# Kernel tuning notes

Hardware: AMD Instinct MI355X
Metric: run time of the kernel (lower is better)

## Reference

```python
import jax, jax.numpy as jnp
import numpy as np

N = 50000    # nodes
E = 800000   # edges (avg degree 16)
H = 4        # attention heads
IN = 128     # input feature size
HID = 128    # hidden size per head
OUT = 64     # output size per head
GAT_SLOPE = 0.2   # DGL GATConv internal LeakyReLU slope
ACT_SLOPE = 0.01  # nn.LeakyReLU default slope


def _lrelu(x, s):
    return jnp.where(x >= 0, x, s * x)


def _gat_conv(x, src, dst, W, attn_l, attn_r, bias, heads, out_dim):
    """DGL GATConv (feat_drop disabled for deterministic reference).
    x: [N, F_in] -> out: [N, heads, out_dim]"""
    z = (x @ W).reshape(N, heads, out_dim)                 # [N,H,D]
    el = jnp.sum(z * attn_l, axis=-1)                      # [N,H]
    er = jnp.sum(z * attn_r, axis=-1)                      # [N,H]
    e = _lrelu(el[src] + er[dst], GAT_SLOPE)               # [E,H]
    # edge softmax over incoming edges of each dst node (numerically stable)
    emax = jax.ops.segment_max(e, dst, num_segments=N)     # [N,H]
    ex = jnp.exp(e - emax[dst])                            # [E,H]
    esum = jax.ops.segment_sum(ex, dst, num_segments=N)    # [N,H]
    alpha = ex / esum[dst]                                 # [E,H]
    msg = alpha[:, :, None] * z[src]                       # [E,H,D]
    out = jax.ops.segment_sum(msg, dst, num_segments=N)    # [N,H,D]
    return out + bias.reshape(1, heads, out_dim)


def setup_inputs() -> dict:
    key = jax.random.key(0)
    ks = jax.random.split(key, 20)
    def nrm(k, shape, scale=0.05):
        return jax.random.normal(k, shape, dtype=jnp.float32) * scale
    return {
        "n_feat": jax.random.normal(ks[0], (N, IN), dtype=jnp.float32),
        "src": jax.random.randint(ks[1], (E,), 0, N),
        "dst": jax.random.randint(ks[2], (E,), 0, N),
        # input GATConv: IN -> HID x H
        "g0_W": nrm(ks[3], (IN, H * HID)),
        "g0_al": nrm(ks[4], (H, HID)),
        "g0_ar": nrm(ks[5], (H, HID)),
        "g0_b": jnp.zeros((H * HID,), jnp.float32),
        "d0_W": nrm(ks[6], (HID, H * HID)),
        "d0_b": jnp.zeros((HID,), jnp.float32),
        # middle GATConv: HID -> HID x H
        "g1_W": nrm(ks[7], (HID, H * HID)),
        "g1_al": nrm(ks[8], (H, HID)),
        "g1_ar": nrm(ks[9], (H, HID)),
        "g1_b": jnp.zeros((H * HID,), jnp.float32),
        "d1_W": nrm(ks[10], (HID, H * HID)),
        "d1_b": jnp.zeros((HID,), jnp.float32),
        # output GATConv: HID -> OUT x H
        "g2_W": nrm(ks[11], (HID, H * OUT)),
        "g2_al": nrm(ks[12], (H, OUT)),
        "g2_ar": nrm(ks[13], (H, OUT)),
        "g2_b": jnp.zeros((H * OUT,), jnp.float32),
    }


def reference(n_feat, src, dst,
              g0_W, g0_al, g0_ar, g0_b, d0_W, d0_b,
              g1_W, g1_al, g1_ar, g1_b, d1_W, d1_b,
              g2_W, g2_al, g2_ar, g2_b):
    # input GAT + dense
    h = _gat_conv(n_feat, src, dst, g0_W, g0_al, g0_ar, g0_b, H, HID)  # [N,H,HID]
    h = _lrelu(h, ACT_SLOPE).reshape(N, H * HID)
    h = _lrelu(h @ d0_W.T + d0_b, ACT_SLOPE)                            # [N,HID]
    # middle GAT + dense
    h = _gat_conv(h, src, dst, g1_W, g1_al, g1_ar, g1_b, H, HID)
    h = _lrelu(h, ACT_SLOPE).reshape(N, H * HID)
    h = _lrelu(h @ d1_W.T + d1_b, ACT_SLOPE)                            # [N,HID]
    # output GAT, mean over heads
    h = _gat_conv(h, src, dst, g2_W, g2_al, g2_ar, g2_b, H, OUT)        # [N,H,OUT]
    h = _lrelu(h, ACT_SLOPE)
    h = jnp.mean(h, axis=-2)                                            # [N,OUT]
    h = _lrelu(h, ACT_SLOPE)
    return h
```

## Files before the change

kernel.cpp:

```cpp
#include <hip/hip_runtime.h>

#define NN 50000
#define EE 800000
#define HH 4

typedef __attribute__((ext_vector_type(8))) short short8v;
typedef __attribute__((ext_vector_type(4))) float f32x4;
typedef __attribute__((ext_vector_type(8))) unsigned short ushort8v;
typedef __attribute__((ext_vector_type(4))) unsigned short ushort4v;

__device__ __forceinline__ float b2f(unsigned short u) {
    return __uint_as_float(((unsigned int)u) << 16);
}
__device__ __forceinline__ unsigned short f2b(float f) {
    unsigned int x = __float_as_uint(f);
    x += 0x7fffu + ((x >> 16) & 1u);
    return (unsigned short)(x >> 16);
}

template<int WR, bool ACT, int WEL>
__global__ __launch_bounds__(256) void mgemm_k(
    const unsigned short* __restrict__ A, const unsigned short* __restrict__ Bt,
    const float* __restrict__ bias, unsigned short* __restrict__ C,
    const float* __restrict__ al, const float* __restrict__ ar,
    float* __restrict__ el, float* __restrict__ er,
    int M, int N, int K, float slope)
{
    constexpr int BM = 64 * WR;
    __shared__ unsigned short As[BM * 72];
    __shared__ unsigned short Bs[128 * 72];
    const int t   = threadIdx.x;
    const int m0  = blockIdx.y * BM;
    const int n0  = blockIdx.x * 128;
    const int w   = t >> 6;
    const int l   = t & 63;
    const int lr  = l & 15;
    const int lk8 = (l >> 4) * 8;
    const int wbase = w * 16 * WR;

    f32x4 acc[WR][8];
    #pragma unroll
    for (int rr = 0; rr < WR; ++rr)
        #pragma unroll
        for (int i = 0; i < 8; ++i) acc[rr][i] = (f32x4)0.f;

    for (int k0 = 0; k0 < K; k0 += 64) {
        #pragma unroll
        for (int cc = 0; cc < 2 * WR; ++cc) {
            int c = t + cc * 256;
            int row = c >> 3, seg = (c & 7) * 8;
            int gm = m0 + row;
            short8v v = (short8v)0;
            if (gm < M)
                v = *reinterpret_cast<const short8v*>(&A[(size_t)gm * K + k0 + seg]);
            *reinterpret_cast<short8v*>(&As[row * 72 + seg]) = v;
        }
        #pragma unroll
        for (int cc = 0; cc < 4; ++cc) {
            int c = t + cc * 256;
            int row = c >> 3, seg = (c & 7) * 8;
            short8v v = *reinterpret_cast<const short8v*>(
                &Bt[(size_t)(n0 + row) * K + k0 + seg]);
            *reinterpret_cast<short8v*>(&Bs[row * 72 + seg]) = v;
        }
        __syncthreads();
        #pragma unroll
        for (int kk = 0; kk < 64; kk += 32) {
            short8v a[WR];
            #pragma unroll
            for (int rr = 0; rr < WR; ++rr)
                a[rr] = *reinterpret_cast<const short8v*>(
                    &As[(wbase + rr * 16 + lr) * 72 + kk + lk8]);
            #pragma unroll
            for (int nb = 0; nb < 8; ++nb) {
                short8v b = *reinterpret_cast<const short8v*>(
                    &Bs[(nb * 16 + lr) * 72 + kk + lk8]);
                #pragma unroll
                for (int rr = 0; rr < WR; ++rr)
                    acc[rr][nb] = __builtin_amdgcn_mfma_f32_16x16x32_bf16(
                        a[rr], b, acc[rr][nb], 0, 0, 0);
            }
        }
        __syncthreads();
    }

    if (WEL > 0) {
        const int nbh = (WEL == 1) ? 8 : 4;
        const int Dd  = (WEL == 1) ? 128 : 64;
        #pragma unroll
        for (int hh = 0; hh < WEL; ++hh) {
            int head = (WEL == 1) ? blockIdx.x : blockIdx.x * 2 + hh;
            #pragma unroll
            for (int rr = 0; rr < WR; ++rr) {
                float pl[4] = {}, pr[4] = {};
                #pragma unroll
                for (int nb = 0; nb < nbh; ++nb) {
                    float alv = al[head * Dd + nb * 16 + lr];
                    float arv = ar[head * Dd + nb * 16 + lr];
                    #pragma unroll
                    for (int r = 0; r < 4; ++r) {
                        float z = acc[rr][hh * nbh + nb][r];
                        pl[r] = fmaf(z, alv, pl[r]);
                        pr[r] = fmaf(z, arv, pr[r]);
                    }
                }
                #pragma unroll
                for (int r = 0; r < 4; ++r) {
                    #pragma unroll
                    for (int o = 1; o < 16; o <<= 1) {
                        pl[r] += __shfl_xor(pl[r], o);
                        pr[r] += __shfl_xor(pr[r], o);
                    }
                }
                if (lr == 0) {
                    #pragma unroll
                    for (int r = 0; r < 4; ++r) {
                        int gm = m0 + wbase + rr * 16 + (l >> 4) * 4 + r;
                        if (gm < M) {
                            el[gm * HH + head] = pl[r];
                            er[gm * HH + head] = pr[r];
                        }
                    }
                }
            }
        }
    }

    #pragma unroll
    for (int rr = 0; rr < WR; ++rr) {
        #pragma unroll
        for (int nb = 0; nb < 8; ++nb) {
            #pragma unroll
            for (int r = 0; r < 4; ++r) {
                int gm = m0 + wbase + rr * 16 + (l >> 4) * 4 + r;
                int gn = n0 + nb * 16 + lr;
                if (gm < M) {
                    float v = acc[rr][nb][r];
                    if (ACT) { v += bias[gn]; v = v >= 0.f ? v : slope * v; }
                    C[(size_t)gm * N + gn] = f2b(v);
                }
            }
        }
    }
}

__global__ void tr_k(const float* __restrict__ W, unsigned short* __restrict__ Wt,
                     int K, int N)
{
    int idx = blockIdx.x * blockDim.x + threadIdx.x;
    if (idx >= K * N) return;
    int n = idx / K, k = idx - n * K;
    Wt[idx] = f2b(W[(size_t)k * N + n]);
}

__global__ void cast_k(const float* __restrict__ x, unsigned short* __restrict__ y,
                       int n4)
{
    int i = blockIdx.x * blockDim.x + threadIdx.x;
    if (i >= n4) return;
    float4 v = reinterpret_cast<const float4*>(x)[i];
    ushort4v u;
    u[0] = f2b(v.x); u[1] = f2b(v.y); u[2] = f2b(v.z); u[3] = f2b(v.w);
    reinterpret_cast<ushort4v*>(y)[i] = u;
}

__global__ void hist_k(const int* __restrict__ dst, int* __restrict__ cnt)
{
    int i = blockIdx.x * blockDim.x + threadIdx.x;
    if (i < EE) atomicAdd(&cnt[dst[i]], 1);
}

#define SCAN_B 196
__global__ __launch_bounds__(256) void scan1_k(const int* __restrict__ cnt,
                                               int* __restrict__ offs,
                                               int* __restrict__ bsum)
{
    __shared__ int sh[256];
    int b = blockIdx.x, t = threadIdx.x, i = b * 256 + t;
    int v = (i < NN) ? cnt[i] : 0;
    sh[t] = v;
    __syncthreads();
    #pragma unroll
    for (int o = 1; o < 256; o <<= 1) {
        int add = (t >= o) ? sh[t - o] : 0;
        __syncthreads();
        sh[t] += add;
        __syncthreads();
    }
    if (i < NN) offs[i] = sh[t] - v;
    if (t == 255) bsum[b] = sh[t];
}

__global__ __launch_bounds__(256) void scan2_k(int* __restrict__ bsum)
{
    __shared__ int sh[256];
    int t = threadIdx.x;
    int v = (t < SCAN_B) ? bsum[t] : 0;
    sh[t] = v;
    __syncthreads();
    #pragma unroll
    for (int o = 1; o < 256; o <<= 1) {
        int add = (t >= o) ? sh[t - o] : 0;
        __syncthreads();
        sh[t] += add;
        __syncthreads();
    }
    if (t < SCAN_B) bsum[t] = sh[t] - v;
}

__global__ __launch_bounds__(256) void scan3_k(int* __restrict__ offs,
                                               const int* __restrict__ bsum)
{
    int b = blockIdx.x, t = threadIdx.x, i = b * 256 + t;
    if (i < NN) offs[i] += bsum[b];
    if (i == NN - 1) offs[NN] = EE;
}

__global__ void scatter_k(const int* __restrict__ src, const int* __restrict__ dst,
                          const int* __restrict__ offs, int* __restrict__ cursor,
                          int* __restrict__ srcs_sorted)
{
    int i = blockIdx.x * blockDim.x + threadIdx.x;
    if (i >= EE) return;
    int d = dst[i];
    int p = offs[d] + atomicAdd(&cursor[d], 1);
    srcs_sorted[p] = src[i];
}

template<int D, bool MEAN>
__global__ __launch_bounds__(256) void agg2_k(
    const unsigned short* __restrict__ zb, const float* __restrict__ el,
    const float* __restrict__ er, const int* __restrict__ offs,
    const int* __restrict__ srcs, const float* __restrict__ bias,
    unsigned short* __restrict__ outb, float* __restrict__ outf)
{
    constexpr int HD  = HH * D;
    constexpr int EPL = HD / 64;
    typedef __attribute__((ext_vector_type(EPL))) unsigned short uvec;
    int n = blockIdx.x * 4 + (threadIdx.x >> 6);
    if (n >= NN) return;
    int lane = threadIdx.x & 63;
    int h = lane >> 4;
    int beg = offs[n];
    int cnt_e = offs[n + 1] - beg;
    float erh = er[n * HH + h];

    float acc[EPL] = {};
    float wsum = 0.f;

    if (cnt_e > 0) {
        auto LD = [&](int idx, uvec& v, float& elv) {
            int e = idx < cnt_e ? idx : cnt_e - 1;
            int s = srcs[beg + e];
            elv = el[s * HH + h];
            v = *reinterpret_cast<const uvec*>(&zb[(size_t)s * HD + lane * EPL]);
        };
        auto PROC = [&](const uvec& v, float elv) {
            float x = elv + erh;
            x = x >= 0.f ? x : 0.2f * x;
            float ex = __expf(x);
            wsum += ex;
            #pragma unroll
            for (int j = 0; j < EPL; ++j)
                acc[j] = fmaf(ex, b2f(v[j]), acc[j]);
        };
        uvec v0, v1, v2, v3;
        float e0, e1, e2, e3;
        LD(0, v0, e0); LD(1, v1, e1); LD(2, v2, e2); LD(3, v3, e3);
        for (int c0 = 0; c0 < cnt_e; c0 += 4) {
            PROC(v0, e0); LD(c0 + 4, v0, e0);
            if (c0 + 1 < cnt_e) { PROC(v1, e1); } LD(c0 + 5, v1, e1);
            if (c0 + 2 < cnt_e) { PROC(v2, e2); } LD(c0 + 6, v2, e2);
            if (c0 + 3 < cnt_e) { PROC(v3, e3); } LD(c0 + 7, v3, e3);
        }
    }
    float inv = wsum > 0.f ? 1.f / wsum : 0.f;

    float vv[EPL];
    #pragma unroll
    for (int j = 0; j < EPL; ++j) {
        float v = acc[j] * inv + bias[h * D + (lane & 15) * EPL + j];
        vv[j] = v >= 0.f ? v : 0.01f * v;
    }

    if (!MEAN) {
        uvec u;
        #pragma unroll
        for (int j = 0; j < EPL; ++j) u[j] = f2b(vv[j]);
        *reinterpret_cast<uvec*>(&outb[(size_t)n * HD + lane * EPL]) = u;
    } else {
        #pragma unroll
        for (int j = 0; j < EPL; ++j) {
            float s = vv[j];
            s += __shfl_xor(s, 16);
            s += __shfl_xor(s, 32);
            s *= 0.25f;
            vv[j] = s >= 0.f ? s : 0.01f * s;
        }
        if (lane < 16) {
            float* op = outf + (size_t)n * D + lane * EPL;
            #pragma unroll
            for (int j = 0; j < EPL; j += 4)
                *reinterpret_cast<float4*>(op + j) =
                    make_float4(vv[j], vv[j + 1], vv[j + 2], vv[j + 3]);
        }
    }
}

extern "C" void kernel_launch(void* const* d_in, const int* in_sizes, int n_in,
                              void* d_out, int out_size, void* d_ws, size_t ws_size,
                              hipStream_t stream)
{
    const float* n_feat = (const float*)d_in[0];
    const int*   src    = (const int*)d_in[1];
    const int*   dst    = (const int*)d_in[2];
    const float* g0_W  = (const float*)d_in[3];
    const float* g0_al = (const float*)d_in[4];
    const float* g0_ar = (const float*)d_in[5];
    const float* g0_b  = (const float*)d_in[6];
    const float* d0_W  = (const float*)d_in[7];
    const float* d0_b  = (const float*)d_in[8];
    const float* g1_W  = (const float*)d_in[9];
    const float* g1_al = (const float*)d_in[10];
    const float* g1_ar = (const float*)d_in[11];
    const float* g1_b  = (const float*)d_in[12];
    const float* d1_W  = (const float*)d_in[13];
    const float* d1_b  = (const float*)d_in[14];
    const float* g2_W  = (const float*)d_in[15];
    const float* g2_al = (const float*)d_in[16];
    const float* g2_ar = (const float*)d_in[17];
    const float* g2_b  = (const float*)d_in[18];

    char* ws = (char*)d_ws;
    size_t off = 0;
    auto alloc = [&](size_t bytes) {
        void* p = ws + off;
        off += (bytes + 255) & ~(size_t)255;
        return p;
    };
    unsigned short* zB   = (unsigned short*)alloc((size_t)NN * 512 * 2);
    unsigned short* hB   = (unsigned short*)alloc((size_t)NN * 512 * 2);
    unsigned short* hC   = (unsigned short*)alloc((size_t)NN * 128 * 2);
    unsigned short* xF   = (unsigned short*)alloc((size_t)NN * 128 * 2);
    unsigned short* g0t  = (unsigned short*)alloc(512 * 128 * 2);
    unsigned short* g1t  = (unsigned short*)alloc(512 * 128 * 2);
    unsigned short* g2t  = (unsigned short*)alloc(256 * 128 * 2);
    unsigned short* d0t  = (unsigned short*)alloc(128 * 512 * 2);
    unsigned short* d1t  = (unsigned short*)alloc(128 * 512 * 2);
    float*          el   = (float*)alloc((size_t)NN * HH * 4);
    float*          er   = (float*)alloc((size_t)NN * HH * 4);
    int*            cnt  = (int*)alloc((size_t)NN * 4);
    int*            curs = (int*)alloc((size_t)NN * 4);
    int*            offs = (int*)alloc((size_t)(NN + 1) * 4);
    int*            srcs = (int*)alloc((size_t)EE * 4);
    int*            bsum = (int*)alloc(256 * 4);

    hipMemsetAsync(cnt, 0, (size_t)NN * 4, stream);
    hipMemsetAsync(curs, 0, (size_t)NN * 4, stream);
    hist_k<<<(EE + 255) / 256, 256, 0, stream>>>(dst, cnt);
    scan1_k<<<SCAN_B, 256, 0, stream>>>(cnt, offs, bsum);
    scan2_k<<<1, 256, 0, stream>>>(bsum);
    scan3_k<<<SCAN_B, 256, 0, stream>>>(offs, bsum);
    scatter_k<<<(EE + 255) / 256, 256, 0, stream>>>(src, dst, offs, curs, srcs);

    cast_k<<<(NN * 128 / 4 + 255) / 256, 256, 0, stream>>>(n_feat, xF, NN * 128 / 4);
    cast_k<<<(128 * 512 / 4 + 255) / 256, 256, 0, stream>>>(d0_W, d0t, 128 * 512 / 4);
    cast_k<<<(128 * 512 / 4 + 255) / 256, 256, 0, stream>>>(d1_W, d1t, 128 * 512 / 4);
    tr_k<<<(128 * 512 + 255) / 256, 256, 0, stream>>>(g0_W, g0t, 128, 512);
    tr_k<<<(128 * 512 + 255) / 256, 256, 0, stream>>>(g1_W, g1t, 128, 512);
    tr_k<<<(128 * 256 + 255) / 256, 256, 0, stream>>>(g2_W, g2t, 128, 256);

    const int MT   = (NN + 63) / 64;
    const int MT2  = (NN + 127) / 128;
    const int NODB = (NN + 3) / 4;

    mgemm_k<2, false, 1><<<dim3(4, MT2), 256, 0, stream>>>(
        xF, g0t, nullptr, zB, g0_al, g0_ar, el, er, NN, 512, 128, 0.f);
    agg2_k<128, false><<<NODB, 256, 0, stream>>>(zB, el, er, offs, srcs, g0_b,
                                                 hB, nullptr);
    mgemm_k<1, true, 0><<<dim3(1, MT), 256, 0, stream>>>(
        hB, d0t, d0_b, hC, nullptr, nullptr, nullptr, nullptr, NN, 128, 512, 0.01f);

    mgemm_k<2, false, 1><<<dim3(4, MT2), 256, 0, stream>>>(
        hC, g1t, nullptr, zB, g1_al, g1_ar, el, er, NN, 512, 128, 0.f);
    agg2_k<128, false><<<NODB, 256, 0, stream>>>(zB, el, er, offs, srcs, g1_b,
                                                 hB, nullptr);
    mgemm_k<1, true, 0><<<dim3(1, MT), 256, 0, stream>>>(
        hB, d1t, d1_b, hC, nullptr, nullptr, nullptr, nullptr, NN, 128, 512, 0.01f);

    mgemm_k<2, false, 2><<<dim3(2, MT2), 256, 0, stream>>>(
        hC, g2t, nullptr, zB, g2_al, g2_ar, el, er, NN, 256, 128, 0.f);
    agg2_k<64, true><<<NODB, 256, 0, stream>>>(zB, el, er, offs, srcs, g2_b,
                                               nullptr, (float*)d_out);
}
```

Measured before the change: 570.7 us.

## Store GAT features head-major and aggregate one head per block for cache locality

The projection GEMM now writes z in a head-major layout [H][N][128] and el/er as [H][N], and the first two aggregations launch a separate grid slice per head. Each wave then gathers 256-byte rows from one head's table. The working set per head is smaller and more likely to stay in L2/MALL while the random neighbour gathers run. In exchange each head pass rereads the CSR offsets and source indices and reruns the exp/softmax weight math separately, and each edge now issues smaller loads.

```diff
diff --git a/kernel.cpp b/kernel.cpp
--- a/kernel.cpp
+++ b/kernel.cpp
@@ -6,7 +6,6 @@
 
 typedef __attribute__((ext_vector_type(8))) short short8v;
 typedef __attribute__((ext_vector_type(4))) float f32x4;
-typedef __attribute__((ext_vector_type(8))) unsigned short ushort8v;
 typedef __attribute__((ext_vector_type(4))) unsigned short ushort4v;
 
 __device__ __forceinline__ float b2f(unsigned short u) {
@@ -18,12 +17,12 @@
     return (unsigned short)(x >> 16);
 }
 
-template<int WR, bool ACT, int WEL>
+template<int WR, bool ACT, int WEL, bool HS>
 __global__ __launch_bounds__(256) void mgemm_k(
     const unsigned short* __restrict__ A, const unsigned short* __restrict__ Bt,
     const float* __restrict__ bias, unsigned short* __restrict__ C,
     const float* __restrict__ al, const float* __restrict__ ar,
-    float* __restrict__ el, float* __restrict__ er,
+    float* __restrict__ elt, float* __restrict__ ert,
     int M, int N, int K, float slope)
 {
     constexpr int BM = 64 * WR;
@@ -117,8 +116,8 @@
                     for (int r = 0; r < 4; ++r) {
                         int gm = m0 + wbase + rr * 16 + (l >> 4) * 4 + r;
                         if (gm < M) {
-                            el[gm * HH + head] = pl[r];
-                            er[gm * HH + head] = pr[r];
+                            elt[(size_t)head * NN + gm] = pl[r];
+                            ert[(size_t)head * NN + gm] = pr[r];
                         }
                     }
                 }
@@ -137,7 +136,13 @@
                 if (gm < M) {
                     float v = acc[rr][nb][r];
                     if (ACT) { v += bias[gn]; v = v >= 0.f ? v : slope * v; }
-                    C[(size_t)gm * N + gn] = f2b(v);
+                    if (HS) {
+                        int head = blockIdx.x;
+                        int d = nb * 16 + lr;
+                        C[((size_t)head * NN + gm) * 128 + d] = f2b(v);
+                    } else {
+                        C[(size_t)gm * N + gn] = f2b(v);
+                    }
                 }
             }
         }
@@ -227,15 +232,64 @@
     srcs_sorted[p] = src[i];
 }
 
-template<int D, bool MEAN>
-__global__ __launch_bounds__(256) void agg2_k(
-    const unsigned short* __restrict__ zb, const float* __restrict__ el,
-    const float* __restrict__ er, const int* __restrict__ offs,
+__global__ __launch_bounds__(256) void agg3_k(
+    const unsigned short* __restrict__ zh, const float* __restrict__ elt,
+    const float* __restrict__ ert, const int* __restrict__ offs,
     const int* __restrict__ srcs, const float* __restrict__ bias,
-    unsigned short* __restrict__ outb, float* __restrict__ outf)
-{
-    constexpr int HD  = HH * D;
-    constexpr int EPL = HD / 64;
+    unsigned short* __restrict__ outb)
+{
+    int n = blockIdx.x * 4 + (threadIdx.x >> 6);
+    if (n >= NN) return;
+    int h = blockIdx.y;
+    int lane = threadIdx.x & 63;
+    int beg = offs[n];
+    int cnt_e = offs[n + 1] - beg;
+    float erh = ert[(size_t)h * NN + n];
+    const unsigned short* ztab = zh + (size_t)h * NN * 128;
+    const float* elh = elt + (size_t)h * NN;
+
+    float a0 = 0.f, a1 = 0.f, wsum = 0.f;
+    if (cnt_e > 0) {
+        auto LD = [&](int idx, unsigned int& v, float& elv) {
+            int e = idx < cnt_e ? idx : cnt_e - 1;
+            int s = srcs[beg + e];
+            elv = elh[s];
+            v = *reinterpret_cast<const unsigned int*>(&ztab[(size_t)s * 128 + lane * 2]);
+        };
+        auto PROC = [&](unsigned int v, float elv) {
+            float x = elv + erh;
+            x = x >= 0.f ? x : 0.2f * x;
+            float ex = __expf(x);
+            wsum += ex;
+            a0 = fmaf(ex, b2f((unsigned short)(v & 0xffff)), a0);
+            a1 = fmaf(ex, b2f((unsigned short)(v >> 16)), a1);
+        };
+        unsigned int v0, v1, v2, v3;
+        float e0, e1, e2, e3;
+        LD(0, v0, e0); LD(1, v1, e1); LD(2, v2, e2); LD(3, v3, e3);
+        for (int c0 = 0; c0 < cnt_e; c0 += 4) {
+            PROC(v0, e0); LD(c0 + 4, v0, e0);
+            if (c0 + 1 < cnt_e) { PROC(v1, e1); } LD(c0 + 5, v1, e1);
+            if (c0 + 2 < cnt_e) { PROC(v2, e2); } LD(c0 + 6, v2, e2);
+            if (c0 + 3 < cnt_e) { PROC(v3, e3); } LD(c0 + 7, v3, e3);
+        }
+    }
+    float inv = wsum > 0.f ? 1.f / wsum : 0.f;
+    float x0 = a0 * inv + bias[h * 128 + lane * 2];
+    float x1 = a1 * inv + bias[h * 128 + lane * 2 + 1];
+    x0 = x0 >= 0.f ? x0 : 0.01f * x0;
+    x1 = x1 >= 0.f ? x1 : 0.01f * x1;
+    unsigned int u = (unsigned int)f2b(x0) | ((unsigned int)f2b(x1) << 16);
+    *reinterpret_cast<unsigned int*>(&outb[(size_t)n * 512 + h * 128 + lane * 2]) = u;
+}
+
+__global__ __launch_bounds__(256) void aggm_k(
+    const unsigned short* __restrict__ zb, const float* __restrict__ elt,
+    const float* __restrict__ ert, const int* __restrict__ offs,
+    const int* __restrict__ srcs, const float* __restrict__ bias,
+    float* __restrict__ outf)
+{
+    constexpr int D = 64, HD = 256, EPL = 4;
     typedef __attribute__((ext_vector_type(EPL))) unsigned short uvec;
     int n = blockIdx.x * 4 + (threadIdx.x >> 6);
     if (n >= NN) return;
@@ -243,16 +297,15 @@
     int h = lane >> 4;
     int beg = offs[n];
     int cnt_e = offs[n + 1] - beg;
-    float erh = er[n * HH + h];
+    float erh = ert[(size_t)h * NN + n];
 
     float acc[EPL] = {};
     float wsum = 0.f;
-
     if (cnt_e > 0) {
         auto LD = [&](int idx, uvec& v, float& elv) {
             int e = idx < cnt_e ? idx : cnt_e - 1;
             int s = srcs[beg + e];
-            elv = el[s * HH + h];
+            elv = elt[(size_t)h * NN + s];
             v = *reinterpret_cast<const uvec*>(&zb[(size_t)s * HD + lane * EPL]);
         };
         auto PROC = [&](const uvec& v, float elv) {
@@ -282,28 +335,18 @@
         float v = acc[j] * inv + bias[h * D + (lane & 15) * EPL + j];
         vv[j] = v >= 0.f ? v : 0.01f * v;
     }
-
-    if (!MEAN) {
-        uvec u;
-        #pragma unroll
-        for (int j = 0; j < EPL; ++j) u[j] = f2b(vv[j]);
-        *reinterpret_cast<uvec*>(&outb[(size_t)n * HD + lane * EPL]) = u;
-    } else {
-        #pragma unroll
-        for (int j = 0; j < EPL; ++j) {
-            float s = vv[j];
-            s += __shfl_xor(s, 16);
-            s += __shfl_xor(s, 32);
-            s *= 0.25f;
-            vv[j] = s >= 0.f ? s : 0.01f * s;
-        }
-        if (lane < 16) {
-            float* op = outf + (size_t)n * D + lane * EPL;
-            #pragma unroll
-            for (int j = 0; j < EPL; j += 4)
-                *reinterpret_cast<float4*>(op + j) =
-                    make_float4(vv[j], vv[j + 1], vv[j + 2], vv[j + 3]);
-        }
+    #pragma unroll
+    for (int j = 0; j < EPL; ++j) {
+        float s = vv[j];
+        s += __shfl_xor(s, 16);
+        s += __shfl_xor(s, 32);
+        s *= 0.25f;
+        vv[j] = s >= 0.f ? s : 0.01f * s;
+    }
+    if (lane < 16) {
+        float* op = outf + (size_t)n * D + lane * EPL;
+        *reinterpret_cast<float4*>(op) =
+            make_float4(vv[0], vv[1], vv[2], vv[3]);
     }
 }
 
@@ -374,22 +417,19 @@
     const int MT2  = (NN + 127) / 128;
     const int NODB = (NN + 3) / 4;
 
-    mgemm_k<2, false, 1><<<dim3(4, MT2), 256, 0, stream>>>(
+    mgemm_k<2, false, 1, true><<<dim3(4, MT2), 256, 0, stream>>>(
         xF, g0t, nullptr, zB, g0_al, g0_ar, el, er, NN, 512, 128, 0.f);
-    agg2_k<128, false><<<NODB, 256, 0, stream>>>(zB, el, er, offs, srcs, g0_b,
-                                                 hB, nullptr);
-    mgemm_k<1, true, 0><<<dim3(1, MT), 256, 0, stream>>>(
+    agg3_k<<<dim3(NODB, HH), 256, 0, stream>>>(zB, el, er, offs, srcs, g0_b, hB);
+    mgemm_k<1, true, 0, false><<<dim3(1, MT), 256, 0, stream>>>(
         hB, d0t, d0_b, hC, nullptr, nullptr, nullptr, nullptr, NN, 128, 512, 0.01f);
 
-    mgemm_k<2, false, 1><<<dim3(4, MT2), 256, 0, stream>>>(
+    mgemm_k<2, false, 1, true><<<dim3(4, MT2), 256, 0, stream>>>(
         hC, g1t, nullptr, zB, g1_al, g1_ar, el, er, NN, 512, 128, 0.f);
-    agg2_k<128, false><<<NODB, 256, 0, stream>>>(zB, el, er, offs, srcs, g1_b,
-                                                 hB, nullptr);
-    mgemm_k<1, true, 0><<<dim3(1, MT), 256, 0, stream>>>(
+    agg3_k<<<dim3(NODB, HH), 256, 0, stream>>>(zB, el, er, offs, srcs, g1_b, hB);
+    mgemm_k<1, true, 0, false><<<dim3(1, MT), 256, 0, stream>>>(
         hB, d1t, d1_b, hC, nullptr, nullptr, nullptr, nullptr, NN, 128, 512, 0.01f);
 
-    mgemm_k<2, false, 2><<<dim3(2, MT2), 256, 0, stream>>>(
+    mgemm_k<2, false, 2, false><<<dim3(2, MT2), 256, 0, stream>>>(
         hC, g2t, nullptr, zB, g2_al, g2_ar, el, er, NN, 256, 128, 0.f);
-    agg2_k<64, true><<<NODB, 256, 0, stream>>>(zB, el, er, offs, srcs, g2_b,
-                                               nullptr, (float*)d_out);
-}
+    aggm_k<<<NODB, 256, 0, stream>>>(zB, el, er, offs, srcs, g2_b, (float*)d_out);
+}
```

New measurement: 705.3 us. 23.6% more time.
